# Kernel tuning notes

Measured on AMD Instinct MI355X. Metric: run time of the kernel, lower is better.

Reference implementation:

```python
import jax, jax.numpy as jnp
from jax import lax
import numpy as np

D_MODEL = 1024
D_INNER = 2048   # expand * d_model
D_STATE = 128
NHEADS = 16
HEADDIM = 128
NGROUPS = 1
D_CONV = 4
CHUNK = 256
CONV_DIM = D_INNER + 2 * NGROUPS * D_STATE  # 2304
DIM_IN_PROJ = 2 * D_INNER + 2 * NGROUPS * D_STATE + NHEADS  # 4368
EPS = 1e-5


def setup_inputs() -> dict:
    key = jax.random.key(0)
    ks = jax.random.split(key, 10)
    u = jax.random.normal(ks[0], (2, 4096, D_MODEL), dtype=jnp.float32)
    W_in = jax.random.normal(ks[1], (DIM_IN_PROJ, D_MODEL), dtype=jnp.float32) * (1.0 / np.sqrt(D_MODEL))
    conv_w = jax.random.normal(ks[2], (CONV_DIM, 1, D_CONV), dtype=jnp.float32) * (1.0 / np.sqrt(D_CONV))
    conv_b = jax.random.normal(ks[3], (CONV_DIM,), dtype=jnp.float32) * 0.02
    # dt init: exp(uniform * (log dt_max - log dt_min) + log dt_min), inverse softplus
    dt = jnp.exp(jax.random.uniform(ks[4], (NHEADS,)) * (np.log(0.02) - np.log(0.001)) + np.log(0.001))
    dt = jnp.clip(dt, 1e-4, None)
    dt_bias = dt + jnp.log(-jnp.expm1(-dt))
    A_log = jnp.log(jax.random.uniform(ks[5], (NHEADS,), minval=1.0, maxval=16.0))
    D = jnp.ones((NHEADS,), dtype=jnp.float32)
    norm_weight = jnp.ones((D_INNER,), dtype=jnp.float32)
    W_out = jax.random.normal(ks[6], (D_MODEL, D_INNER), dtype=jnp.float32) * (1.0 / np.sqrt(D_INNER))
    return {"u": u, "W_in": W_in, "conv_w": conv_w, "conv_b": conv_b,
            "dt_bias": dt_bias, "A_log": A_log, "D": D,
            "norm_weight": norm_weight, "W_out": W_out}


def _segsum(x):
    # x: (..., T) -> (..., T, T); out[i, j] = sum_{k=j+1..i} x_k for j <= i, else -inf
    T = x.shape[-1]
    cs = jnp.cumsum(x, axis=-1)
    seg = cs[..., :, None] - cs[..., None, :]
    mask = jnp.tril(jnp.ones((T, T), dtype=bool))
    return jnp.where(mask, seg, -jnp.inf)


def _mamba2_forward(u, W_in, conv_w, conv_b, dt_bias, A_log, D, norm_weight, W_out):
    b, L, _ = u.shape
    zxbcdt = u @ W_in.T  # (b, L, 4368)
    z = zxbcdt[..., :D_INNER]
    xBC = zxbcdt[..., D_INNER:D_INNER + CONV_DIM]
    dt = zxbcdt[..., D_INNER + CONV_DIM:]  # (b, L, h)

    # causal depthwise conv1d + SiLU
    xBC_t = xBC.transpose(0, 2, 1)  # (b, d, L)
    conv = lax.conv_general_dilated(xBC_t, conv_w, (1,), [(D_CONV - 1, 0)],
                                    feature_group_count=CONV_DIM,
                                    dimension_numbers=("NCW", "OIW", "NCW"))
    xBC = jax.nn.silu((conv + conv_b[None, :, None]).transpose(0, 2, 1))

    x = xBC[..., :D_INNER].reshape(b, L, NHEADS, HEADDIM)
    Bm = xBC[..., D_INNER:D_INNER + D_STATE]          # ngroups = 1
    Cm = xBC[..., D_INNER + D_STATE:]

    dt = jax.nn.softplus(dt + dt_bias)  # (b, L, h)
    A = -jnp.exp(A_log)                 # (h,)

    nc = L // CHUNK
    xc = x.reshape(b, nc, CHUNK, NHEADS, HEADDIM)
    dtc = dt.reshape(b, nc, CHUNK, NHEADS)
    Bc = Bm.reshape(b, nc, CHUNK, D_STATE)
    Cc = Cm.reshape(b, nc, CHUNK, D_STATE)

    dA = (dtc * A).transpose(0, 1, 3, 2)        # (b, c, h, q)
    A_cs = jnp.cumsum(dA, axis=-1)              # (b, c, h, q)
    Lmat = jnp.exp(_segsum(dA))                 # (b, c, h, q, q)
    xdt = xc * dtc[..., None]                   # (b, c, q, h, p)

    # intra-chunk (diagonal block) output
    CB = jnp.einsum("bcqn,bcsn->bcqs", Cc, Bc)
    Y_diag = jnp.einsum("bcqs,bchqs,bcshp->bcqhp", CB, Lmat, xdt)

    # per-chunk final states
    decay_states = jnp.exp(A_cs[..., -1:] - A_cs)  # (b, c, h, q)
    states = jnp.einsum("bcqn,bchq,bcqhp->bchpn", Bc, decay_states, xdt)

    # inter-chunk recurrence over chunk axis (small: nc steps)
    chunk_decay = jnp.exp(A_cs[..., -1])  # (b, c, h)
    def step(carry, inp):
        dec, s = inp
        return carry * dec[..., None, None] + s, carry
    init = jnp.zeros_like(states[:, 0])
    _, prev = lax.scan(step, init,
                       (chunk_decay.transpose(1, 0, 2), states.transpose(1, 0, 2, 3, 4)))
    prev = prev.transpose(1, 0, 2, 3, 4)  # (b, c, h, p, n) state entering each chunk

    Y_off = jnp.einsum("bcqn,bchpn,bchq->bcqhp", Cc, prev, jnp.exp(A_cs))

    y = (Y_diag + Y_off).reshape(b, L, NHEADS, HEADDIM) + D[None, None, :, None] * x
    y = y.reshape(b, L, D_INNER)

    # gated RMSNorm (norm_before_gate=False): norm(y * silu(z)) * weight
    y = y * jax.nn.silu(z)
    y = y * lax.rsqrt(jnp.mean(y * y, axis=-1, keepdims=True) + EPS) * norm_weight

    return y @ W_out.T


def reference(u, W_in, conv_w, conv_b, dt_bias, A_log, D, norm_weight, W_out):
    return _mamba2_forward(u, W_in, conv_w, conv_b, dt_bias, A_log, D, norm_weight, W_out)
```

## Files before the change

kernel.cpp:

```cpp
#include <hip/hip_runtime.h>
#include <hip/hip_bf16.h>
#include <cstddef>
#include <cstdint>

#define D_MODEL     1024
#define D_INNER     2048
#define D_STATE     128
#define NHEADS      16
#define HEADDIM     128
#define D_CONV      4
#define CHUNK       256
#define CONV_DIM    2304
#define DIM_IN_PROJ 4368
#define NPAD_WIN    4608
#define BATCH       2
#define SEQ         4096
#define ROWS        8192
#define NC          16
#define EPS         1e-5f

typedef __hip_bfloat16 bf16;
typedef __attribute__((ext_vector_type(8))) short bf16x8;
typedef __attribute__((ext_vector_type(4))) float f32x4;

__device__ __forceinline__ float sigmoidf_(float x) { return 1.f / (1.f + expf(-x)); }

__device__ __forceinline__ float ldf(const float* p) { return *p; }
__device__ __forceinline__ float ldf(const bf16* p)  { return __bfloat162float(*p); }
__device__ __forceinline__ void  stf(float* p, float v) { *p = v; }
__device__ __forceinline__ void  stf(bf16* p, float v)  { *p = __float2bfloat16(v); }

__device__ __forceinline__ short f2bs(float x) {
    bf16 h = __float2bfloat16(x);
    return __builtin_bit_cast(short, h);
}
__device__ __forceinline__ float bs2f(short s) {
    unsigned int u = ((unsigned int)(unsigned short)s) << 16;
    return __builtin_bit_cast(float, u);
}

#define GLOAD_LDS16(gp, lp) \
    __builtin_amdgcn_global_load_lds((const __attribute__((address_space(1))) unsigned int*)(gp), \
        (__attribute__((address_space(3))) unsigned int*)(lp), 16, 0, 0)

__global__ __launch_bounds__(512, 1) void gemm256_mfma_bt(
    const bf16* __restrict__ A, const bf16* __restrict__ B, bf16* __restrict__ C,
    int M, int N, int K, int lda, int ldb, int ldc, int gx)
{
    __shared__ bf16 As[2][2][256 * 32];
    __shared__ bf16 Bs[2][2][256 * 32];

    const int tid  = threadIdx.x;
    const int lane = tid & 63;
    const int wave = tid >> 6;
    const int wm   = wave >> 2;
    const int wn   = wave & 3;
    const int l15  = lane & 15;
    const int l4   = lane >> 4;

    const int cpx  = (int)gridDim.x >> 3;
    const int wg   = ((int)blockIdx.x & 7) * cpx + ((int)blockIdx.x >> 3);
    const int row0 = (wg / gx) * 256;
    const int col0 = (wg % gx) * 256;

    const int NT = K >> 6;

    f32x4 acc[8][4];
#pragma unroll
    for (int m = 0; m < 8; m++)
#pragma unroll
        for (int n = 0; n < 4; n++) acc[m][n] = (f32x4){0.f, 0.f, 0.f, 0.f};

#define BAR_()  { asm volatile("" ::: "memory"); __builtin_amdgcn_s_barrier(); asm volatile("" ::: "memory"); }
#define VMW0_() asm volatile("s_waitcnt vmcnt(0)" ::: "memory")
#define VMW4_() asm volatile("s_waitcnt vmcnt(4)" ::: "memory")

    auto STAGE_A = [&](int kt, int buf, int kk) {
#pragma unroll
        for (int sw = 0; sw < 2; sw++) {
            int s  = sw * 512 + tid;
            int r  = s >> 2;
            int cg = (s & 3) ^ ((r >> 1) & 3);
            const bf16* src = A + (size_t)(row0 + r) * lda + kt * 64 + kk * 32 + cg * 8;
            GLOAD_LDS16(src, &As[buf][kk][s * 8]);
        }
    };
    auto STAGE_B = [&](int kt, int buf, int kk) {
#pragma unroll
        for (int sw = 0; sw < 2; sw++) {
            int s  = sw * 512 + tid;
            int r  = s >> 2;
            int cg = (s & 3) ^ ((r >> 1) & 3);
            const bf16* src = B + (size_t)(col0 + r) * ldb + kt * 64 + kk * 32 + cg * 8;
            GLOAD_LDS16(src, &Bs[buf][kk][s * 8]);
        }
    };
    auto LOADA = [&](int buf, int mq, int kk, bf16x8* af) {
#pragma unroll
        for (int i = 0; i < 4; i++) {
            int r = wm * 128 + (mq * 4 + i) * 16 + l15;
            af[i] = *reinterpret_cast<const bf16x8*>(
                &As[buf][kk][r * 32 + ((l4 ^ ((r >> 1) & 3)) << 3)]);
        }
    };
    auto LOADB = [&](int buf, int kk, bf16x8* bb) {
#pragma unroll
        for (int n = 0; n < 4; n++) {
            int r = wn * 64 + n * 16 + l15;
            bb[n] = *reinterpret_cast<const bf16x8*>(
                &Bs[buf][kk][r * 32 + ((l4 ^ ((r >> 1) & 3)) << 3)]);
        }
    };
    auto MFMAQ = [&](int mq, bf16x8* af, bf16x8* bb) {
        __builtin_amdgcn_s_setprio(1);
#pragma unroll
        for (int i = 0; i < 4; i++)
#pragma unroll
            for (int n = 0; n < 4; n++)
                acc[mq * 4 + i][n] = __builtin_amdgcn_mfma_f32_16x16x32_bf16(
                    af[i], bb[n], acc[mq * 4 + i][n], 0, 0, 0);
        __builtin_amdgcn_s_setprio(0);
    };

    STAGE_A(0, 0, 0); STAGE_B(0, 0, 0);
    STAGE_A(0, 0, 1); STAGE_B(0, 0, 1);
    VMW0_();
    BAR_();

    bf16x8 af[4], bb[4];
    for (int t = 0; t < NT; t++) {
        const int buf  = t & 1;
        const int nbuf = buf ^ 1;
        const int nk   = (t + 1 < NT) ? t + 1 : 0;
        LOADA(buf, 0, 0, af);
        LOADB(buf, 0, bb);
        STAGE_A(nk, nbuf, 0);
        MFMAQ(0, af, bb);
        LOADA(buf, 1, 0, af);
        STAGE_B(nk, nbuf, 0);
        VMW4_();
        BAR_();
        MFMAQ(1, af, bb);
        LOADA(buf, 0, 1, af);
        LOADB(buf, 1, bb);
        STAGE_A(nk, nbuf, 1);
        MFMAQ(0, af, bb);
        LOADA(buf, 1, 1, af);
        STAGE_B(nk, nbuf, 1);
        VMW4_();
        BAR_();
        MFMAQ(1, af, bb);
    }

#pragma unroll
    for (int m = 0; m < 8; m++) {
        int gr = row0 + wm * 128 + m * 16 + l4 * 4;
#pragma unroll
        for (int n = 0; n < 4; n++) {
            int gc = col0 + wn * 64 + n * 16 + l15;
            if (gc < N) {
#pragma unroll
                for (int j = 0; j < 4; j++)
                    stf(&C[(size_t)(gr + j) * ldc + gc], acc[m][n][j]);
            }
        }
    }
#undef BAR_
#undef VMW0_
#undef VMW4_
}

template<typename TC>
__global__ __launch_bounds__(256, 2) void gemm128c_mfma_bt(
    const bf16* __restrict__ A, const bf16* __restrict__ B, TC* __restrict__ C,
    int M, int N, int K, int lda, int ldb, int ldc, int gx)
{
    __shared__ bf16 As[2][2][128 * 32];
    __shared__ bf16 Bs[2][2][128 * 32];

    const int tid  = threadIdx.x;
    const int lane = tid & 63;
    const int wave = tid >> 6;
    const int wm   = wave >> 1;
    const int wn   = wave & 1;
    const int l15  = lane & 15;
    const int l4   = lane >> 4;

    const int cpx  = (int)gridDim.x >> 3;
    const int wg   = ((int)blockIdx.x & 7) * cpx + ((int)blockIdx.x >> 3);
    const int row0 = (wg / gx) * 128;
    const int col0 = (wg % gx) * 128;

    const int NT = K >> 6;

    f32x4 acc[4][4];
#pragma unroll
    for (int m = 0; m < 4; m++)
#pragma unroll
        for (int n = 0; n < 4; n++) acc[m][n] = (f32x4){0.f, 0.f, 0.f, 0.f};

#define BAR_()  { asm volatile("" ::: "memory"); __builtin_amdgcn_s_barrier(); asm volatile("" ::: "memory"); }
#define VMW0_() asm volatile("s_waitcnt vmcnt(0)" ::: "memory")
#define VMW4_() asm volatile("s_waitcnt vmcnt(4)" ::: "memory")

    auto STAGE_A = [&](int kt, int buf, int kk) {
#pragma unroll
        for (int sw = 0; sw < 2; sw++) {
            int s  = sw * 256 + tid;
            int r  = s >> 2;
            int cg = (s & 3) ^ ((r >> 1) & 3);
            const bf16* src = A + (size_t)(row0 + r) * lda + kt * 64 + kk * 32 + cg * 8;
            GLOAD_LDS16(src, &As[buf][kk][s * 8]);
        }
    };
    auto STAGE_B = [&](int kt, int buf, int kk) {
#pragma unroll
        for (int sw = 0; sw < 2; sw++) {
            int s  = sw * 256 + tid;
            int r  = s >> 2;
            int cg = (s & 3) ^ ((r >> 1) & 3);
            const bf16* src = B + (size_t)(col0 + r) * ldb + kt * 64 + kk * 32 + cg * 8;
            GLOAD_LDS16(src, &Bs[buf][kk][s * 8]);
        }
    };
    auto LOADA = [&](int buf, int kk, bf16x8* af) {
#pragma unroll
        for (int i = 0; i < 4; i++) {
            int r = wm * 64 + i * 16 + l15;
            af[i] = *reinterpret_cast<const bf16x8*>(
                &As[buf][kk][r * 32 + ((l4 ^ ((r >> 1) & 3)) << 3)]);
        }
    };
    auto LOADB = [&](int buf, int kk, bf16x8* bb) {
#pragma unroll
        for (int n = 0; n < 4; n++) {
            int r = wn * 64 + n * 16 + l15;
            bb[n] = *reinterpret_cast<const bf16x8*>(
                &Bs[buf][kk][r * 32 + ((l4 ^ ((r >> 1) & 3)) << 3)]);
        }
    };
    auto MFMAQ = [&](bf16x8* af, bf16x8* bb) {
        __builtin_amdgcn_s_setprio(1);
#pragma unroll
        for (int i = 0; i < 4; i++)
#pragma unroll
            for (int n = 0; n < 4; n++)
                acc[i][n] = __builtin_amdgcn_mfma_f32_16x16x32_bf16(
                    af[i], bb[n], acc[i][n], 0, 0, 0);
        __builtin_amdgcn_s_setprio(0);
    };

    STAGE_A(0, 0, 0); STAGE_B(0, 0, 0);
    STAGE_A(0, 0, 1); STAGE_B(0, 0, 1);
    VMW0_();
    BAR_();

    bf16x8 af[4], bb[4];
    for (int t = 0; t < NT; t++) {
        const int buf  = t & 1;
        const int nbuf = buf ^ 1;
        const int nk   = (t + 1 < NT) ? t + 1 : 0;
        LOADA(buf, 0, af);
        LOADB(buf, 0, bb);
        STAGE_A(nk, nbuf, 0);
        STAGE_B(nk, nbuf, 0);
        VMW4_();
        BAR_();
        MFMAQ(af, bb);
        LOADA(buf, 1, af);
        LOADB(buf, 1, bb);
        STAGE_A(nk, nbuf, 1);
        STAGE_B(nk, nbuf, 1);
        VMW4_();
        BAR_();
        MFMAQ(af, bb);
    }

#pragma unroll
    for (int m = 0; m < 4; m++) {
        int gr = row0 + wm * 64 + m * 16 + l4 * 4;
#pragma unroll
        for (int n = 0; n < 4; n++) {
            int gc = col0 + wn * 64 + n * 16 + l15;
            if (gc < N) {
#pragma unroll
                for (int j = 0; j < 4; j++)
                    stf(&C[(size_t)(gr + j) * ldc + gc], acc[m][n][j]);
            }
        }
    }
#undef BAR_
#undef VMW0_
#undef VMW4_
}

template<typename TC>
__global__ __launch_bounds__(256) void gemm_mfma_bt(
    const bf16* __restrict__ A, const bf16* __restrict__ B, TC* __restrict__ C,
    int M, int N, int K, int lda, int ldb, int ldc,
    long long sA, long long sB, long long sC)
{
    A += (long long)blockIdx.z * sA;
    B += (long long)blockIdx.z * sB;
    C += (long long)blockIdx.z * sC;

    __shared__ bf16 As[128 * 32];
    __shared__ bf16 Bs[128 * 32];

    const int tid  = threadIdx.x;
    const int lane = tid & 63;
    const int wave = tid >> 6;
    const int wr   = wave >> 1;
    const int wc   = wave & 1;
    const int row0 = blockIdx.y * 128;
    const int col0 = blockIdx.x * 128;
    const int l15  = lane & 15;
    const int l4   = lane >> 4;

    const int srow = tid >> 2;
    const int scol = (tid & 3) * 8;

    f32x4 acc[4][4];
#pragma unroll
    for (int m = 0; m < 4; m++)
#pragma unroll
        for (int n = 0; n < 4; n++) acc[m][n] = (f32x4){0.f, 0.f, 0.f, 0.f};

    for (int k0 = 0; k0 < K; k0 += 32) {
        const bf16* gA0 = A + (size_t)(row0 + srow) * lda + k0 + scol;
        const bf16* gA1 = A + (size_t)(row0 + 64 + srow) * lda + k0 + scol;
        const bf16* gB0 = B + (size_t)(col0 + srow) * ldb + k0 + scol;
        const bf16* gB1 = B + (size_t)(col0 + 64 + srow) * ldb + k0 + scol;
        GLOAD_LDS16(gA0, &As[tid * 8]);
        GLOAD_LDS16(gA1, &As[2048 + tid * 8]);
        GLOAD_LDS16(gB0, &Bs[tid * 8]);
        GLOAD_LDS16(gB1, &Bs[2048 + tid * 8]);
        __syncthreads();

        bf16x8 af[4], bg[4];
#pragma unroll
        for (int m = 0; m < 4; m++) {
            int r = wr * 64 + m * 16 + l15;
            af[m] = *reinterpret_cast<const bf16x8*>(&As[r * 32 + l4 * 8]);
        }
#pragma unroll
        for (int n = 0; n < 4; n++) {
            int r = wc * 64 + n * 16 + l15;
            bg[n] = *reinterpret_cast<const bf16x8*>(&Bs[r * 32 + l4 * 8]);
        }
#pragma unroll
        for (int m = 0; m < 4; m++)
#pragma unroll
            for (int n = 0; n < 4; n++)
                acc[m][n] = __builtin_amdgcn_mfma_f32_16x16x32_bf16(af[m], bg[n], acc[m][n], 0, 0, 0);
        __syncthreads();
    }

#pragma unroll
    for (int m = 0; m < 4; m++) {
        int grb = row0 + wr * 64 + m * 16 + l4 * 4;
#pragma unroll
        for (int n = 0; n < 4; n++) {
            int gc = col0 + wc * 64 + n * 16 + l15;
            if (gc < N) {
#pragma unroll
                for (int j = 0; j < 4; j++) {
                    int gr = grb + j;
                    if (gr < M) stf(&C[(size_t)gr * ldc + gc], acc[m][n][j]);
                }
            }
        }
    }
}

__global__ __launch_bounds__(256) void dt_proj_kernel(
    const float* __restrict__ u, const float* __restrict__ Wdt,
    const float* __restrict__ dt_bias, float* __restrict__ dtsp,
    ushort* __restrict__ ub)
{
    const int wave = threadIdx.x >> 6;
    const int lane = threadIdx.x & 63;
    const int row  = blockIdx.x * 4 + wave;
    const float* urow = u + (size_t)row * D_MODEL;

    float4 uv[4];
#pragma unroll
    for (int w = 0; w < 4; w++)
        uv[w] = *reinterpret_cast<const float4*>(&urow[lane * 4 + w * 256]);

#pragma unroll
    for (int w = 0; w < 4; w++) {
        ushort4 o;
        o.x = (unsigned short)f2bs(uv[w].x);
        o.y = (unsigned short)f2bs(uv[w].y);
        o.z = (unsigned short)f2bs(uv[w].z);
        o.w = (unsigned short)f2bs(uv[w].w);
        *reinterpret_cast<ushort4*>(&ub[(size_t)row * D_MODEL + lane * 4 + w * 256]) = o;
    }

    float acc[NHEADS];
#pragma unroll
    for (int h = 0; h < NHEADS; h++) acc[h] = 0.f;
#pragma unroll
    for (int w = 0; w < 4; w++) {
#pragma unroll
        for (int h = 0; h < NHEADS; h++) {
            float4 wv = *reinterpret_cast<const float4*>(&Wdt[(size_t)h * D_MODEL + lane * 4 + w * 256]);
            acc[h] += uv[w].x * wv.x + uv[w].y * wv.y + uv[w].z * wv.z + uv[w].w * wv.w;
        }
    }
#pragma unroll
    for (int h = 0; h < NHEADS; h++)
#pragma unroll
        for (int off = 32; off > 0; off >>= 1)
            acc[h] += __shfl_xor(acc[h], off, 64);

    float sel = 0.f;
#pragma unroll
    for (int h = 0; h < NHEADS; h++) sel = (lane == h) ? acc[h] : sel;
    if (lane < NHEADS) {
        float x = sel + dt_bias[lane];
        dtsp[(size_t)row * NHEADS + lane] = (x > 20.f) ? x : log1pf(expf(x));
    }
}

__global__ __launch_bounds__(256) void cast_bf16_kernel(
    const float4* __restrict__ src, ushort4* __restrict__ dst, int n4)
{
    int i = blockIdx.x * 256 + threadIdx.x;
    if (i >= n4) return;
    float4 v = src[i];
    ushort4 o;
    o.x = (unsigned short)f2bs(v.x);
    o.y = (unsigned short)f2bs(v.y);
    o.z = (unsigned short)f2bs(v.z);
    o.w = (unsigned short)f2bs(v.w);
    dst[i] = o;
}

__global__ __launch_bounds__(256) void cast_win_kernel(
    const float4* __restrict__ src, ushort4* __restrict__ dst)
{
    int i = blockIdx.x * 256 + threadIdx.x;
    if (i >= NPAD_WIN * D_MODEL / 4) return;
    int row = (i * 4) / D_MODEL;
    ushort4 o = {0, 0, 0, 0};
    if (row < DIM_IN_PROJ) {
        float4 v = src[i];
        o.x = (unsigned short)f2bs(v.x);
        o.y = (unsigned short)f2bs(v.y);
        o.z = (unsigned short)f2bs(v.z);
        o.w = (unsigned short)f2bs(v.w);
    }
    dst[i] = o;
}

__global__ __launch_bounds__(256) void conv_silu_kernel(
    const bf16* __restrict__ zx, const float* __restrict__ cw,
    const float* __restrict__ cb, bf16* __restrict__ xbc)
{
    const int CW = CONV_DIM / 8;
    int idx = blockIdx.x * 256 + threadIdx.x;
    if (idx >= (ROWS / 4) * CW) return;
    int c8   = idx % CW;
    int r4   = idx / CW;
    int c0   = c8 * 8;
    int row0 = r4 * 4;
    int l0   = row0 & (SEQ - 1);

    float vr[7][8];
#pragma unroll
    for (int k = 0; k < 7; k++) {
        int ls = l0 - 3 + k;
        if (ls < 0) {
#pragma unroll
            for (int j = 0; j < 8; j++) vr[k][j] = 0.f;
        } else {
            bf16x8 v = *reinterpret_cast<const bf16x8*>(
                zx + (size_t)(row0 - 3 + k) * DIM_IN_PROJ + D_INNER + c0);
#pragma unroll
            for (int j = 0; j < 8; j++) vr[k][j] = bs2f(v[j]);
        }
    }

    float4 t[8];
#pragma unroll
    for (int j = 0; j < 8; j++)
        t[j] = *reinterpret_cast<const float4*>(&cw[(size_t)(c0 + j) * D_CONV]);
    float bias[8];
    {
        float4 b0 = *reinterpret_cast<const float4*>(&cb[c0]);
        float4 b1 = *reinterpret_cast<const float4*>(&cb[c0 + 4]);
        bias[0] = b0.x; bias[1] = b0.y; bias[2] = b0.z; bias[3] = b0.w;
        bias[4] = b1.x; bias[5] = b1.y; bias[6] = b1.z; bias[7] = b1.w;
    }

#pragma unroll
    for (int r = 0; r < 4; r++) {
        float acc[8];
#pragma unroll
        for (int j = 0; j < 8; j++) acc[j] = bias[j];
#pragma unroll
        for (int k = 0; k < D_CONV; k++) {
#pragma unroll
            for (int j = 0; j < 8; j++) {
                float tap = (k == 0) ? t[j].x : (k == 1) ? t[j].y : (k == 2) ? t[j].z : t[j].w;
                acc[j] += tap * vr[r + k][j];
            }
        }
        bf16x8 o;
#pragma unroll
        for (int j = 0; j < 8; j++) {
            float x = acc[j];
            o[j] = f2bs(x * sigmoidf_(x));
        }
        *reinterpret_cast<bf16x8*>(&xbc[(size_t)(row0 + r) * CONV_DIM + c0]) = o;
    }
}

__global__ __launch_bounds__(256) void cumsum_kernel(
    const float* __restrict__ dtsp, const float* __restrict__ A_log,
    float* __restrict__ Acs)
{
    int blk = blockIdx.x;
    int h   = blk % NHEADS;
    int bc  = blk / NHEADS;
    int t   = threadIdx.x;
    int row = bc * CHUNK + t;
    float A = -expf(A_log[h]);
    __shared__ float buf[CHUNK];
    buf[t] = dtsp[(size_t)row * NHEADS + h] * A;
    __syncthreads();
    for (int off = 1; off < CHUNK; off <<= 1) {
        float v = (t >= off) ? buf[t - off] : 0.f;
        __syncthreads();
        buf[t] += v;
        __syncthreads();
    }
    Acs[(size_t)blk * CHUNK + t] = buf[t];
}

__global__ __launch_bounds__(256, 2) void states_mfma_kernel(
    const bf16* __restrict__ xbc, const float* __restrict__ dtsp,
    const float* __restrict__ Acs, float* __restrict__ states)
{
    const int bch  = blockIdx.x;
    const int h    = bch % NHEADS;
    const int bc   = bch / NHEADS;
    const int row0 = bc * CHUNK;
    const int tid  = threadIdx.x;
    const int lane = tid & 63;
    const int wave = tid >> 6;
    const int l15  = lane & 15;
    const int l4   = lane >> 4;

    __shared__ float g[CHUNK];
    __shared__ bf16 xT[128 * 32];
    __shared__ bf16 bT[128 * 32];

    {
        float last = Acs[(size_t)bch * CHUNK + CHUNK - 1];
        float a    = Acs[(size_t)bch * CHUNK + tid];
        g[tid] = dtsp[(size_t)(row0 + tid) * NHEADS + h] * __expf(last - a);
    }

    const int sp0 = (tid & 15) * 8;
    const int ssl = 2 * (tid >> 4);

    f32x4 acc[2][8];
#pragma unroll
    for (int m = 0; m < 2; m++)
#pragma unroll
        for (int n = 0; n < 8; n++) acc[m][n] = (f32x4){0.f, 0.f, 0.f, 0.f};

    for (int q0 = 0; q0 < CHUNK; q0 += 32) {
        __syncthreads();
        {
            const bf16* gx = xbc + (size_t)(row0 + q0 + ssl) * CONV_DIM + h * HEADDIM + sp0;
            bf16x8 v0 = *reinterpret_cast<const bf16x8*>(gx);
            bf16x8 v1 = *reinterpret_cast<const bf16x8*>(gx + CONV_DIM);
            const bf16* gb = xbc + (size_t)(row0 + q0 + ssl) * CONV_DIM + D_INNER + sp0;
            bf16x8 w0 = *reinterpret_cast<const bf16x8*>(gb);
            bf16x8 w1 = *reinterpret_cast<const bf16x8*>(gb + CONV_DIM);
            float g0 = g[q0 + ssl], g1 = g[q0 + ssl + 1];
#pragma unroll
            for (int j = 0; j < 8; j++) {
                unsigned int px = (unsigned short)f2bs(bs2f(v0[j]) * g0) |
                                  ((unsigned int)(unsigned short)f2bs(bs2f(v1[j]) * g1) << 16);
                *reinterpret_cast<unsigned int*>(&xT[(sp0 + j) * 32 + ssl]) = px;
                unsigned int pb = (unsigned short)w0[j] |
                                  ((unsigned int)(unsigned short)w1[j] << 16);
                *reinterpret_cast<unsigned int*>(&bT[(sp0 + j) * 32 + ssl]) = pb;
            }
        }
        __syncthreads();

        bf16x8 af[2], bg[8];
#pragma unroll
        for (int m = 0; m < 2; m++) {
            int p = wave * 32 + m * 16 + l15;
            af[m] = *reinterpret_cast<const bf16x8*>(&xT[p * 32 + l4 * 8]);
        }
#pragma unroll
        for (int n = 0; n < 8; n++) {
            int nn = n * 16 + l15;
            bg[n] = *reinterpret_cast<const bf16x8*>(&bT[nn * 32 + l4 * 8]);
        }
#pragma unroll
        for (int m = 0; m < 2; m++)
#pragma unroll
            for (int n = 0; n < 8; n++)
                acc[m][n] = __builtin_amdgcn_mfma_f32_16x16x32_bf16(af[m], bg[n], acc[m][n], 0, 0, 0);
    }

    float* sp = states + (size_t)bch * HEADDIM * D_STATE;
#pragma unroll
    for (int m = 0; m < 2; m++) {
        int pb = wave * 32 + m * 16 + l4 * 4;
#pragma unroll
        for (int n = 0; n < 8; n++) {
            int nn = n * 16 + l15;
#pragma unroll
            for (int j = 0; j < 4; j++)
                sp[(size_t)(pb + j) * D_STATE + nn] = acc[m][n][j];
        }
    }
}

__global__ __launch_bounds__(256) void chunkscan_kernel(
    float* __restrict__ states, const float* __restrict__ Acs)
{
    int idx = blockIdx.x * 256 + threadIdx.x;
    int pn  = idx % (HEADDIM * D_STATE);
    int bh  = idx / (HEADDIM * D_STATE);
    int h   = bh % NHEADS;
    int b   = bh / NHEADS;
    float carry = 0.f;
    for (int c = 0; c < NC; c++) {
        int bch = (b * NC + c) * NHEADS + h;
        size_t off = (size_t)bch * HEADDIM * D_STATE + pn;
        float s   = states[off];
        states[off] = carry;
        float dec = expf(Acs[(size_t)bch * CHUNK + CHUNK - 1]);
        carry = carry * dec + s;
    }
}

__global__ __launch_bounds__(256, 2) void y_mfma_kernel(
    const bf16* __restrict__ xbc, const float* __restrict__ dtsp,
    const float* __restrict__ Acs, const float* __restrict__ CBm,
    const float* __restrict__ prev, bf16* __restrict__ Y)
{
    const int bch  = blockIdx.x;
    const int h    = bch % NHEADS;
    const int bc   = bch / NHEADS;
    const int row0 = bc * CHUNK;
    const int tid  = threadIdx.x;
    const int lane = tid & 63;
    const int wave = tid >> 6;
    const int l15  = lane & 15;
    const int l4   = lane >> 4;

    __shared__ float sAcs[CHUNK];
    __shared__ float sdt[CHUNK];
    __shared__ bf16 xT[128 * 32];

    sAcs[tid] = Acs[(size_t)bch * CHUNK + tid];
    sdt[tid]  = dtsp[(size_t)(row0 + tid) * NHEADS + h];
    __syncthreads();

    int qb[4]; float aq[4];
#pragma unroll
    for (int m = 0; m < 4; m++) {
        qb[m] = (m * 4 + wave) * 16;
        aq[m] = sAcs[qb[m] + l15];
    }

    f32x4 acc[4][8];
#pragma unroll
    for (int m = 0; m < 4; m++)
#pragma unroll
        for (int n = 0; n < 8; n++) acc[m][n] = (f32x4){0.f, 0.f, 0.f, 0.f};

    const int sp0 = (tid & 15) * 8;
    const int ssl = 2 * (tid >> 4);

    for (int s0 = 0; s0 < CHUNK; s0 += 32) {
        __syncthreads();
        {
            const bf16* gx = xbc + (size_t)(row0 + s0 + ssl) * CONV_DIM + h * HEADDIM + sp0;
            bf16x8 v0 = *reinterpret_cast<const bf16x8*>(gx);
            bf16x8 v1 = *reinterpret_cast<const bf16x8*>(gx + CONV_DIM);
            float d0 = sdt[s0 + ssl], d1 = sdt[s0 + ssl + 1];
#pragma unroll
            for (int j = 0; j < 8; j++) {
                unsigned int px = (unsigned short)f2bs(bs2f(v0[j]) * d0) |
                                  ((unsigned int)(unsigned short)f2bs(bs2f(v1[j]) * d1) << 16);
                *reinterpret_cast<unsigned int*>(&xT[(sp0 + j) * 32 + ssl]) = px;
            }
        }
        __syncthreads();

        bf16x8 bg[8];
#pragma unroll
        for (int n = 0; n < 8; n++)
            bg[n] = *reinterpret_cast<const bf16x8*>(&xT[(n * 16 + l15) * 32 + l4 * 8]);

        f32x4 as0 = *reinterpret_cast<const f32x4*>(&sAcs[s0 + l4 * 8]);
        f32x4 as1 = *reinterpret_cast<const f32x4*>(&sAcs[s0 + l4 * 8 + 4]);

#pragma unroll
        for (int m = 0; m < 4; m++) {
            if (s0 >= qb[m] + 16) continue;
            int q = qb[m] + l15;
            const float* cbp = CBm + ((size_t)bc * CHUNK + q) * CHUNK + s0 + l4 * 8;
            f32x4 c0 = *reinterpret_cast<const f32x4*>(cbp);
            f32x4 c1 = *reinterpret_cast<const f32x4*>(cbp + 4);
            bf16x8 af;
#pragma unroll
            for (int j = 0; j < 8; j++) {
                int s = s0 + l4 * 8 + j;
                float cb = (j < 4) ? c0[j] : c1[j - 4];
                float a  = (j < 4) ? as0[j] : as1[j - 4];
                float w  = (s <= q) ? cb * __expf(aq[m] - a) : 0.f;
                af[j] = f2bs(w);
            }
#pragma unroll
            for (int n = 0; n < 8; n++)
                acc[m][n] = __builtin_amdgcn_mfma_f32_16x16x32_bf16(af, bg[n], acc[m][n], 0, 0, 0);
        }
    }

    float eaq[4];
#pragma unroll
    for (int m = 0; m < 4; m++) eaq[m] = __expf(aq[m]);

    const float* prevh = prev + (size_t)bch * HEADDIM * D_STATE;
    for (int n0 = 0; n0 < D_STATE; n0 += 32) {
        bf16x8 bg[8];
#pragma unroll
        for (int n = 0; n < 8; n++) {
            const float* pr = prevh + (size_t)(n * 16 + l15) * D_STATE + n0 + l4 * 8;
            f32x4 u0 = *reinterpret_cast<const f32x4*>(pr);
            f32x4 u1 = *reinterpret_cast<const f32x4*>(pr + 4);
            bf16x8 b;
#pragma unroll
            for (int j = 0; j < 4; j++) { b[j] = f2bs(u0[j]); b[4 + j] = f2bs(u1[j]); }
            bg[n] = b;
        }
#pragma unroll
        for (int m = 0; m < 4; m++) {
            const bf16* crow = xbc + (size_t)(row0 + qb[m] + l15) * CONV_DIM
                             + D_INNER + D_STATE + n0 + l4 * 8;
            bf16x8 cv = *reinterpret_cast<const bf16x8*>(crow);
            bf16x8 af;
#pragma unroll
            for (int j = 0; j < 8; j++) af[j] = f2bs(bs2f(cv[j]) * eaq[m]);
#pragma unroll
            for (int n = 0; n < 8; n++)
                acc[m][n] = __builtin_amdgcn_mfma_f32_16x16x32_bf16(af, bg[n], acc[m][n], 0, 0, 0);
        }
    }

#pragma unroll
    for (int m = 0; m < 4; m++) {
        int qrb = qb[m] + l4 * 4;
#pragma unroll
        for (int n = 0; n < 8; n++) {
            int p = n * 16 + l15;
#pragma unroll
            for (int j = 0; j < 4; j++)
                stf(&Y[(size_t)(row0 + qrb + j) * D_INNER + h * HEADDIM + p], acc[m][n][j]);
        }
    }
}

__global__ __launch_bounds__(256) void gate_norm_kernel(
    bf16* __restrict__ Yio, const bf16* __restrict__ zx,
    const bf16* __restrict__ xbc, const float* __restrict__ Dv,
    const float* __restrict__ nw)
{
    int row = blockIdx.x;
    int t   = threadIdx.x;
    int d0  = t * 8;

    bf16x8 yv = *reinterpret_cast<const bf16x8*>(&Yio[(size_t)row * D_INNER + d0]);
    bf16x8 xv = *reinterpret_cast<const bf16x8*>(&xbc[(size_t)row * CONV_DIM + d0]);
    bf16x8 zv = *reinterpret_cast<const bf16x8*>(&zx[(size_t)row * DIM_IN_PROJ + d0]);
    float Dh = Dv[d0 >> 7];

    float vals[8];
    float ss = 0.f;
#pragma unroll
    for (int j = 0; j < 8; j++) {
        float y = bs2f(yv[j]) + Dh * bs2f(xv[j]);
        float z = bs2f(zv[j]);
        y *= z * sigmoidf_(z);
        vals[j] = y;
        ss += y * y;
    }
    __shared__ float red[256];
    red[t] = ss;
    __syncthreads();
    for (int o = 128; o > 0; o >>= 1) {
        if (t < o) red[t] += red[t + o];
        __syncthreads();
    }
    float rms = rsqrtf(red[0] / (float)D_INNER + EPS);

    float4 w0 = *reinterpret_cast<const float4*>(&nw[d0]);
    float4 w1 = *reinterpret_cast<const float4*>(&nw[d0 + 4]);
    bf16x8 o;
    o[0] = f2bs(vals[0] * rms * w0.x);
    o[1] = f2bs(vals[1] * rms * w0.y);
    o[2] = f2bs(vals[2] * rms * w0.z);
    o[3] = f2bs(vals[3] * rms * w0.w);
    o[4] = f2bs(vals[4] * rms * w1.x);
    o[5] = f2bs(vals[5] * rms * w1.y);
    o[6] = f2bs(vals[6] * rms * w1.z);
    o[7] = f2bs(vals[7] * rms * w1.w);
    *reinterpret_cast<bf16x8*>(&Yio[(size_t)row * D_INNER + d0]) = o;
}

extern "C" void kernel_launch(void* const* d_in, const int* in_sizes, int n_in,
                              void* d_out, int out_size, void* d_ws, size_t ws_size,
                              hipStream_t stream)
{
    const float* u       = (const float*)d_in[0];
    const float* W_in    = (const float*)d_in[1];
    const float* conv_w  = (const float*)d_in[2];
    const float* conv_b  = (const float*)d_in[3];
    const float* dt_bias = (const float*)d_in[4];
    const float* A_log   = (const float*)d_in[5];
    const float* Dv      = (const float*)d_in[6];
    const float* norm_w  = (const float*)d_in[7];
    const float* W_out   = (const float*)d_in[8];
    float* out = (float*)d_out;

    char* base = (char*)d_ws;
    size_t off = 0;
    auto alloc = [&](size_t bytes) -> char* {
        char* p = base + off;
        off += (bytes + 255) & ~(size_t)255;
        return p;
    };
    bf16*  zxb    = (bf16*) alloc((size_t)ROWS * DIM_IN_PROJ * 2);
    bf16*  xbc    = (bf16*) alloc((size_t)ROWS * CONV_DIM * 2);
    float* dtsp   = (float*)alloc((size_t)ROWS * NHEADS * 4);
    float* Acs    = (float*)alloc((size_t)BATCH * NC * NHEADS * CHUNK * 4);
    float* states = (float*)alloc((size_t)BATCH * NC * NHEADS * HEADDIM * D_STATE * 4);
    float* CBm    = (float*)alloc((size_t)BATCH * NC * CHUNK * CHUNK * 4);
    bf16*  Y      = (bf16*) alloc((size_t)ROWS * D_INNER * 2);
    bf16*  woutb  = (bf16*) alloc((size_t)D_MODEL * D_INNER * 2);
    bf16*  ub     = Y;
    bf16*  winb   = Y + (size_t)ROWS * D_MODEL;
    if (off > ws_size) return;

    dt_proj_kernel<<<ROWS / 4, 256, 0, stream>>>(
        u, W_in + (size_t)(D_INNER + CONV_DIM) * D_MODEL, dt_bias, dtsp, (ushort*)ub);

    cast_win_kernel<<<(NPAD_WIN * D_MODEL / 4 + 255) / 256, 256, 0, stream>>>(
        (const float4*)W_in, (ushort4*)winb);
    cast_bf16_kernel<<<(D_MODEL * D_INNER / 4 + 255) / 256, 256, 0, stream>>>(
        (const float4*)W_out, (ushort4*)woutb, D_MODEL * D_INNER / 4);

    gemm256_mfma_bt<<<(ROWS / 256) * (NPAD_WIN / 256), 512, 0, stream>>>(
        ub, winb, zxb, ROWS, DIM_IN_PROJ, D_MODEL,
        D_MODEL, D_MODEL, DIM_IN_PROJ, NPAD_WIN / 256);

    conv_silu_kernel<<<((ROWS / 4) * (CONV_DIM / 8)) / 256, 256, 0, stream>>>(
        zxb, conv_w, conv_b, xbc);

    cumsum_kernel<<<BATCH * NC * NHEADS, 256, 0, stream>>>(dtsp, A_log, Acs);

    states_mfma_kernel<<<BATCH * NC * NHEADS, 256, 0, stream>>>(xbc, dtsp, Acs, states);

    chunkscan_kernel<<<(BATCH * NHEADS * HEADDIM * D_STATE) / 256, 256, 0, stream>>>(
        states, Acs);

    gemm_mfma_bt<float><<<dim3(2, 2, BATCH * NC), 256, 0, stream>>>(
        xbc + D_INNER + D_STATE, xbc + D_INNER, CBm,
        CHUNK, CHUNK, D_STATE, CONV_DIM, CONV_DIM, CHUNK,
        (long long)CHUNK * CONV_DIM, (long long)CHUNK * CONV_DIM, (long long)CHUNK * CHUNK);

    y_mfma_kernel<<<BATCH * NC * NHEADS, 256, 0, stream>>>(xbc, dtsp, Acs, CBm, states, Y);

    gate_norm_kernel<<<ROWS, 256, 0, stream>>>(Y, zxb, xbc, Dv, norm_w);

    gemm128c_mfma_bt<float><<<(ROWS / 128) * (D_MODEL / 128), 256, 0, stream>>>(
        Y, woutb, out, ROWS, D_MODEL, D_INNER, D_INNER, D_INNER, D_MODEL, D_MODEL / 128);
}
```

Measured before the change: 336.5 us.

## Replace 256x256 in_proj GEMM with 128x256 tile, two blocks per CU

The input-projection GEMM moves from a 256x256 tile with 512 threads and one block per CU to a 128x256 tile with 256 threads and two blocks per CU. Each step now stages a K=32 slice instead of K=64. The hand-interleaved pipeline with partial vmcnt waits is replaced by a simpler double buffer: wait for all loads, barrier, read LDS, issue the next stage, then run the MFMAs. The goal is more blocks and occupancy to hide latency, at the cost of less data reuse per tile, twice as many barriers per K, and weaker overlap of loads with compute.

Measured after the change: 338.6 us (median of 2 runs). About the same (+0.6%).

```diff
diff --git a/kernel.cpp b/kernel.cpp
--- a/kernel.cpp
+++ b/kernel.cpp
@@ -43,27 +43,25 @@
     __builtin_amdgcn_global_load_lds((const __attribute__((address_space(1))) unsigned int*)(gp), \
         (__attribute__((address_space(3))) unsigned int*)(lp), 16, 0, 0)
 
-__global__ __launch_bounds__(512, 1) void gemm256_mfma_bt(
+__global__ __launch_bounds__(256, 2) void gemm128x256_mfma_bt(
     const bf16* __restrict__ A, const bf16* __restrict__ B, bf16* __restrict__ C,
     int M, int N, int K, int lda, int ldb, int ldc, int gx)
 {
-    __shared__ bf16 As[2][2][256 * 32];
-    __shared__ bf16 Bs[2][2][256 * 32];
+    __shared__ bf16 As[2][128 * 32];
+    __shared__ bf16 Bs[2][256 * 32];
 
     const int tid  = threadIdx.x;
     const int lane = tid & 63;
     const int wave = tid >> 6;
-    const int wm   = wave >> 2;
-    const int wn   = wave & 3;
     const int l15  = lane & 15;
     const int l4   = lane >> 4;
 
     const int cpx  = (int)gridDim.x >> 3;
     const int wg   = ((int)blockIdx.x & 7) * cpx + ((int)blockIdx.x >> 3);
-    const int row0 = (wg / gx) * 256;
+    const int row0 = (wg / gx) * 128;
     const int col0 = (wg % gx) * 256;
 
-    const int NT = K >> 6;
+    const int NT = K >> 5;
 
     f32x4 acc[8][4];
 #pragma unroll
@@ -73,91 +71,76 @@
 
 #define BAR_()  { asm volatile("" ::: "memory"); __builtin_amdgcn_s_barrier(); asm volatile("" ::: "memory"); }
 #define VMW0_() asm volatile("s_waitcnt vmcnt(0)" ::: "memory")
-#define VMW4_() asm volatile("s_waitcnt vmcnt(4)" ::: "memory")
-
-    auto STAGE_A = [&](int kt, int buf, int kk) {
+
+    auto STAGE_A = [&](int kt, int buf) {
 #pragma unroll
         for (int sw = 0; sw < 2; sw++) {
-            int s  = sw * 512 + tid;
+            int s  = sw * 256 + tid;
             int r  = s >> 2;
             int cg = (s & 3) ^ ((r >> 1) & 3);
-            const bf16* src = A + (size_t)(row0 + r) * lda + kt * 64 + kk * 32 + cg * 8;
-            GLOAD_LDS16(src, &As[buf][kk][s * 8]);
-        }
-    };
-    auto STAGE_B = [&](int kt, int buf, int kk) {
-#pragma unroll
-        for (int sw = 0; sw < 2; sw++) {
-            int s  = sw * 512 + tid;
+            const bf16* src = A + (size_t)(row0 + r) * lda + kt * 32 + cg * 8;
+            GLOAD_LDS16(src, &As[buf][s * 8]);
+        }
+    };
+    auto STAGE_B = [&](int kt, int buf) {
+#pragma unroll
+        for (int sw = 0; sw < 4; sw++) {
+            int s  = sw * 256 + tid;
             int r  = s >> 2;
             int cg = (s & 3) ^ ((r >> 1) & 3);
-            const bf16* src = B + (size_t)(col0 + r) * ldb + kt * 64 + kk * 32 + cg * 8;
-            GLOAD_LDS16(src, &Bs[buf][kk][s * 8]);
-        }
-    };
-    auto LOADA = [&](int buf, int mq, int kk, bf16x8* af) {
-#pragma unroll
-        for (int i = 0; i < 4; i++) {
-            int r = wm * 128 + (mq * 4 + i) * 16 + l15;
+            const bf16* src = B + (size_t)(col0 + r) * ldb + kt * 32 + cg * 8;
+            GLOAD_LDS16(src, &Bs[buf][s * 8]);
+        }
+    };
+    auto LOADA = [&](int buf, bf16x8* af) {
+#pragma unroll
+        for (int i = 0; i < 8; i++) {
+            int r = i * 16 + l15;
             af[i] = *reinterpret_cast<const bf16x8*>(
-                &As[buf][kk][r * 32 + ((l4 ^ ((r >> 1) & 3)) << 3)]);
-        }
-    };
-    auto LOADB = [&](int buf, int kk, bf16x8* bb) {
+                &As[buf][r * 32 + ((l4 ^ ((r >> 1) & 3)) << 3)]);
+        }
+    };
+    auto LOADB = [&](int buf, bf16x8* bb) {
 #pragma unroll
         for (int n = 0; n < 4; n++) {
-            int r = wn * 64 + n * 16 + l15;
+            int r = wave * 64 + n * 16 + l15;
             bb[n] = *reinterpret_cast<const bf16x8*>(
-                &Bs[buf][kk][r * 32 + ((l4 ^ ((r >> 1) & 3)) << 3)]);
-        }
-    };
-    auto MFMAQ = [&](int mq, bf16x8* af, bf16x8* bb) {
+                &Bs[buf][r * 32 + ((l4 ^ ((r >> 1) & 3)) << 3)]);
+        }
+    };
+    auto MFMAQ = [&](bf16x8* af, bf16x8* bb) {
         __builtin_amdgcn_s_setprio(1);
 #pragma unroll
-        for (int i = 0; i < 4; i++)
+        for (int i = 0; i < 8; i++)
 #pragma unroll
             for (int n = 0; n < 4; n++)
-                acc[mq * 4 + i][n] = __builtin_amdgcn_mfma_f32_16x16x32_bf16(
-                    af[i], bb[n], acc[mq * 4 + i][n], 0, 0, 0);
+                acc[i][n] = __builtin_amdgcn_mfma_f32_16x16x32_bf16(
+                    af[i], bb[n], acc[i][n], 0, 0, 0);
         __builtin_amdgcn_s_setprio(0);
     };
 
-    STAGE_A(0, 0, 0); STAGE_B(0, 0, 0);
-    STAGE_A(0, 0, 1); STAGE_B(0, 0, 1);
-    VMW0_();
-    BAR_();
-
-    bf16x8 af[4], bb[4];
+    STAGE_A(0, 0); STAGE_B(0, 0);
+
+    bf16x8 af[8], bb[4];
     for (int t = 0; t < NT; t++) {
-        const int buf  = t & 1;
-        const int nbuf = buf ^ 1;
-        const int nk   = (t + 1 < NT) ? t + 1 : 0;
-        LOADA(buf, 0, 0, af);
-        LOADB(buf, 0, bb);
-        STAGE_A(nk, nbuf, 0);
-        MFMAQ(0, af, bb);
-        LOADA(buf, 1, 0, af);
-        STAGE_B(nk, nbuf, 0);
-        VMW4_();
+        const int buf = t & 1;
+        VMW0_();
         BAR_();
-        MFMAQ(1, af, bb);
-        LOADA(buf, 0, 1, af);
-        LOADB(buf, 1, bb);
-        STAGE_A(nk, nbuf, 1);
-        MFMAQ(0, af, bb);
-        LOADA(buf, 1, 1, af);
-        STAGE_B(nk, nbuf, 1);
-        VMW4_();
-        BAR_();
-        MFMAQ(1, af, bb);
+        LOADA(buf, af);
+        LOADB(buf, bb);
+        if (t + 1 < NT) {
+            STAGE_A(t + 1, buf ^ 1);
+            STAGE_B(t + 1, buf ^ 1);
+        }
+        MFMAQ(af, bb);
     }
 
 #pragma unroll
     for (int m = 0; m < 8; m++) {
-        int gr = row0 + wm * 128 + m * 16 + l4 * 4;
+        int gr = row0 + m * 16 + l4 * 4;
 #pragma unroll
         for (int n = 0; n < 4; n++) {
-            int gc = col0 + wn * 64 + n * 16 + l15;
+            int gc = col0 + wave * 64 + n * 16 + l15;
             if (gc < N) {
 #pragma unroll
                 for (int j = 0; j < 4; j++)
@@ -167,7 +150,6 @@
     }
 #undef BAR_
 #undef VMW0_
-#undef VMW4_
 }
 
 template<typename TC>
@@ -864,7 +846,7 @@
     cast_bf16_kernel<<<(D_MODEL * D_INNER / 4 + 255) / 256, 256, 0, stream>>>(
         (const float4*)W_out, (ushort4*)woutb, D_MODEL * D_INNER / 4);
 
-    gemm256_mfma_bt<<<(ROWS / 256) * (NPAD_WIN / 256), 512, 0, stream>>>(
+    gemm128x256_mfma_bt<<<(ROWS / 128) * (NPAD_WIN / 256), 256, 0, stream>>>(
         ub, winb, zxb, ROWS, DIM_IN_PROJ, D_MODEL,
         D_MODEL, D_MODEL, DIM_IN_PROJ, NPAD_WIN / 256);
 
```
